# Performance work log

Measured on AMD Instinct MI355X. Metric: run time of the kernel, lower is better.

The kernel has to match this reference:

```python
import jax, jax.numpy as jnp
import numpy as np

N, B, E, H, G, L = 128, 2, 512, 1024, 50, 3
RBF_RADIUS = 12.0
AVG_LEN = 60.0


def _resmlp(h, Win, bin_, Wh, bh, Wout, bout):
    # input proj + activation, residual hidden blocks, linear head
    h = jax.nn.gelu(h @ Win + bin_, approximate=False)
    for i in range(Wh.shape[0]):  # fixed small number of layers
        h = h + jax.nn.gelu(h @ Wh[i] + bh[i], approximate=False)
    return h @ Wout + bout


def setup_inputs() -> dict:
    key = jax.random.key(0)
    ks = jax.random.split(key, 20)
    s_in = 1.0 / np.sqrt(3 * E)
    s_h = 1.0 / np.sqrt(H)
    s_g = 1.0 / np.sqrt(G)
    return {
        'x': jax.random.normal(ks[0], (N, B, E), jnp.float32),
        'dist': jax.random.uniform(ks[1], (N, N, B), jnp.float32),
        'vec_hat': jax.random.normal(ks[2], (N, N, B, 3), jnp.float32),
        'mask': jnp.ones((B, N), dtype=bool),
        'rbf_W': jax.random.normal(ks[3], (G, E), jnp.float32) * s_g,
        'rbf_b': jnp.zeros((E,), jnp.float32),
        'e_Win': jax.random.normal(ks[4], (3 * E, H), jnp.float32) * s_in,
        'e_bin': jnp.zeros((H,), jnp.float32),
        'e_Wh': jax.random.normal(ks[5], (L, H, H), jnp.float32) * s_h,
        'e_bh': jnp.zeros((L, H), jnp.float32),
        'e_Wout': jax.random.normal(ks[6], (H, 1), jnp.float32) * s_h,
        'e_bout': jnp.zeros((1,), jnp.float32),
        'f_Win': jax.random.normal(ks[7], (3 * E, H), jnp.float32) * s_in,
        'f_bin': jnp.zeros((H,), jnp.float32),
        'f_Wh': jax.random.normal(ks[8], (L, H, H), jnp.float32) * s_h,
        'f_bh': jnp.zeros((L, H), jnp.float32),
        'f_Wout': jax.random.normal(ks[9], (H, 1), jnp.float32) * s_h,
        'f_bout': jnp.zeros((1,), jnp.float32),
    }


def reference(x, dist, vec_hat, mask, rbf_W, rbf_b, e_Win, e_bin, e_Wh, e_bh,
              e_Wout, e_bout, f_Win, f_bin, f_Wh, f_bh, f_Wout, f_bout):
    # Gaussian RBF expansion + linear projection to embed_dim
    offset = jnp.linspace(0.0, RBF_RADIUS, G)
    coeff = -0.5 / (offset[1] - offset[0]) ** 2
    g = jnp.exp(coeff * (dist[..., None] - offset) ** 2)       # (N,N,B,G)
    rbf = g @ rbf_W + rbf_b                                    # (N,N,B,E)

    # all-pairs concat feature: [x_i, x_j, rbf_ij]  -> (N,N,B,3E)
    feat = jnp.concatenate([
        jnp.broadcast_to(x[:, None], rbf.shape),
        jnp.broadcast_to(x[None, :], rbf.shape),
        rbf,
    ], axis=-1)

    entries = (mask.T[:, None] & mask.T[None, :])[..., None].astype(feat.dtype)  # (N,N,B,1)

    energy_pairs = _resmlp(feat, e_Win, e_bin, e_Wh, e_bh, e_Wout, e_bout)       # (N,N,B,1)
    force_pairs = _resmlp(feat, f_Win, f_bin, f_Wh, f_bh, f_Wout, f_bout) * vec_hat  # (N,N,B,3)

    energy = (energy_pairs * entries).sum((0, 1)) / AVG_LEN ** 2  # (B,1)
    forces = (force_pairs * entries).sum(0) / AVG_LEN             # (N,B,3)
    # torch: forces.transpose(0,1)[mask]; mask is all-True here, so this is a reshape
    forces = jnp.swapaxes(forces, 0, 1).reshape(-1, 3)            # (B*N,3)
    return energy, forces
```

## Files before the change

### kernel.cpp

```cpp
#include <hip/hip_runtime.h>
#include <stdint.h>

typedef __bf16 bf16x8 __attribute__((ext_vector_type(8)));
typedef __bf16 bf16x4 __attribute__((ext_vector_type(4)));
typedef float  f32x4  __attribute__((ext_vector_type(4)));
typedef unsigned int u32;

__device__ __forceinline__ void gl_lds16(const void* gptr, void* lptr) {
    __builtin_amdgcn_global_load_lds(
        (const __attribute__((address_space(1))) u32*)gptr,
        (__attribute__((address_space(3))) u32*)lptr,
        16, 0, 0);
}

__device__ __forceinline__ float gelu_f(float x) {
    float u = 0.7978845608f * x * (1.0f + 0.044715f * x * x);
    float e = __expf(2.0f * u);
    float t = 1.0f - 2.0f / (e + 1.0f);
    return 0.5f * x * (1.0f + t);
}

#define MEMFENCE __asm__ __volatile__("" ::: "memory")

__global__ void zero_out(float* __restrict__ o, int n) {
    int i = blockIdx.x * 256 + threadIdx.x;
    if (i < n) o[i] = 0.0f;
}

__global__ __launch_bounds__(256)
void transpose_multi(const float* __restrict__ src0, const float* __restrict__ src1,
                     __bf16* __restrict__ dst0, __bf16* __restrict__ dst1,
                     int K, int Ncols, int perBranch) {
    const int z = blockIdx.z;
    const int branch = z / perBranch;
    const int l = z - branch * perBranch;
    const size_t elems = (size_t)K * Ncols;
    const float* src = (branch ? src1 : src0) + (size_t)l * elems;
    __bf16* dst = (branch ? dst1 : dst0) + (size_t)l * elems;

    __shared__ float tile[64][65];
    const int bk = blockIdx.x * 64;
    const int bn = blockIdx.y * 64;
    const int tid = threadIdx.x;
    const int tr = tid >> 4;
    const int tc = (tid & 15) * 4;
#pragma unroll
    for (int p = 0; p < 4; ++p) {
        const int r = tr + p * 16;
        float4 v = *(const float4*)&src[(size_t)(bk + r) * Ncols + bn + tc];
        tile[r][tc] = v.x; tile[r][tc + 1] = v.y;
        tile[r][tc + 2] = v.z; tile[r][tc + 3] = v.w;
    }
    __syncthreads();
#pragma unroll
    for (int p = 0; p < 4; ++p) {
        const int rn = tr + p * 16;
        bf16x4 o;
        o[0] = (__bf16)tile[tc + 0][rn];
        o[1] = (__bf16)tile[tc + 1][rn];
        o[2] = (__bf16)tile[tc + 2][rn];
        o[3] = (__bf16)tile[tc + 3][rn];
        *(bf16x4*)&dst[(size_t)(bn + rn) * K + bk + tc] = o;
    }
}

__global__ void f32_to_bf16(const float* __restrict__ s, __bf16* __restrict__ d, int n) {
    int idx = blockIdx.x * 256 + threadIdx.x;
    if (idx * 4 < n) {
        float4 v = *(const float4*)(s + idx * 4);
        bf16x4 o;
        o[0] = (__bf16)v.x; o[1] = (__bf16)v.y; o[2] = (__bf16)v.z; o[3] = (__bf16)v.w;
        *(bf16x4*)(d + idx * 4) = o;
    }
}

__global__ void build_M1(const float* __restrict__ rbfW, const float* __restrict__ rbf_b,
                         __bf16* __restrict__ M1) {
    int t = blockIdx.x * 256 + threadIdx.x;
    int r = t >> 8;
    int c = (t & 255) * 2;
    float v0 = 0.f, v1 = 0.f;
    if (r < 50)       { v0 = rbfW[r * 512 + c]; v1 = rbfW[r * 512 + c + 1]; }
    else if (r == 50) { v0 = rbf_b[c];          v1 = rbf_b[c + 1]; }
    M1[r * 512 + c] = (__bf16)v0;
    M1[r * 512 + c + 1] = (__bf16)v1;
}

__global__ __launch_bounds__(256)
void build_G(const float* __restrict__ dist, __bf16* __restrict__ G) {
    const int t = threadIdx.x;
    const int row = blockIdx.x * 32 + (t >> 3);
    const int c0 = (t & 7) * 8;
    const float sp = 12.0f / 49.0f;
    const float coeff = -0.5f / (sp * sp);
    const float d = dist[row];
    bf16x8 v;
#pragma unroll
    for (int q = 0; q < 8; ++q) {
        const int k = c0 + q;
        float val;
        if (k < 50)       { float tt = d - (float)k * sp; val = __expf(coeff * tt * tt); }
        else if (k == 50) val = 1.0f;
        else              val = 0.0f;
        v[q] = (__bf16)val;
    }
    *(bf16x8*)(G + (size_t)row * 64 + c0) = v;
}

template <int NK, int NBN, int MODE, bool DUAL, int MINW, bool SWZ>
__global__ __launch_bounds__(256, MINW)
void gemm_k(const __bf16* __restrict__ A0, const __bf16* __restrict__ A1,
            const __bf16* __restrict__ B0, const __bf16* __restrict__ B1,
            int lda, int ldb, int ldc,
            const float* __restrict__ bias0, const float* __restrict__ bias1,
            __bf16* __restrict__ C0, __bf16* __restrict__ C1,
            float* __restrict__ Cf0, float* __restrict__ Cf1,
            const float* __restrict__ P0, const float* __restrict__ P1,
            const float* __restrict__ wout0, const float* __restrict__ wout1,
            float* __restrict__ dot0, float* __restrict__ dot1) {
    constexpr int NBS = (NBN == 16) ? 4 : (NBN == 8) ? 3 : 0;
    __shared__ __align__(16) __bf16 As[3][128 * 32];
    __shared__ __align__(16) __bf16 Bs[3][128 * 32];

    const int tid = threadIdx.x;
    int bn, bm, branch = 0;
    if constexpr (SWZ) {
        const int x = blockIdx.x & 7;
        const int slot = blockIdx.x >> 3;
        bn = slot & (NBN - 1);
        int grp = x + ((slot >> NBS) << 3);
        if constexpr (DUAL) {
            const int half = (gridDim.x >> NBS) >> 1;
            branch = (grp >= half);
            if (branch) grp -= half;
        }
        bm = grp;
    } else {
        int f2 = blockIdx.x;
        if constexpr (DUAL) {
            const int half = gridDim.x >> 1;
            branch = (f2 >= half);
            if (branch) f2 -= half;
        }
        bn = f2 & (NBN - 1);
        bm = f2 >> NBS;
    }
    const int w = tid >> 6;
    const int lane = tid & 63;

    const __bf16* Ab = (DUAL && branch) ? A1 : A0;
    const __bf16* Bb = (DUAL && branch) ? B1 : B0;

    const int r0 = tid >> 2;
    const int s0 = tid & 3;
    const char* gA0 = (const char*)Ab + (size_t)(bm * 128 + r0) * lda + s0 * 16;
    const char* gA1 = gA0 + (size_t)64 * lda;
    const char* gB0 = (const char*)Bb + (size_t)(bn * 128 + r0) * ldb + s0 * 16;
    const char* gB1 = gB0 + (size_t)64 * ldb;

    char* lA0 = (char*)&As[0][0] + w * 1024;
    char* lA1 = (char*)&As[1][0] + w * 1024;
    char* lA2 = (char*)&As[2][0] + w * 1024;
    char* lB0 = (char*)&Bs[0][0] + w * 1024;
    char* lB1 = (char*)&Bs[1][0] + w * 1024;
    char* lB2 = (char*)&Bs[2][0] + w * 1024;

    const int wm = (w >> 1) & 1;
    const int wn = w & 1;
    const int lm = lane & 15;
    const int ko = (lane >> 4) << 3;
    const int fo = (wm * 64 + lm) * 32 + ko;
    const int go = (wn * 64 + lm) * 32 + ko;
    const __bf16* pA0 = &As[0][0] + fo;
    const __bf16* pA1 = &As[1][0] + fo;
    const __bf16* pA2 = &As[2][0] + fo;
    const __bf16* pB0 = &Bs[0][0] + go;
    const __bf16* pB1 = &Bs[1][0] + go;
    const __bf16* pB2 = &Bs[2][0] + go;

    f32x4 acc[4][4];
    const f32x4 zero = {0.0f, 0.0f, 0.0f, 0.0f};
#pragma unroll
    for (int i = 0; i < 4; ++i)
#pragma unroll
        for (int j = 0; j < 4; ++j) acc[i][j] = zero;

    auto stage = [&](int buf) {
        char* la = (buf == 0) ? lA0 : (buf == 1) ? lA1 : lA2;
        char* lb = (buf == 0) ? lB0 : (buf == 1) ? lB1 : lB2;
        gl_lds16(gA0, la); gl_lds16(gA1, la + 4096);
        gl_lds16(gB0, lb); gl_lds16(gB1, lb + 4096);
        gA0 += 64; gA1 += 64; gB0 += 64; gB1 += 64;
    };
    auto compute = [&](int buf) {
        const __bf16* pa = (buf == 0) ? pA0 : (buf == 1) ? pA1 : pA2;
        const __bf16* pb = (buf == 0) ? pB0 : (buf == 1) ? pB1 : pB2;
        bf16x8 af[4], bfg[4];
#pragma unroll
        for (int i = 0; i < 4; ++i) {
            af[i]  = *(const bf16x8*)(pa + i * 512);
            bfg[i] = *(const bf16x8*)(pb + i * 512);
        }
#pragma unroll
        for (int mi = 0; mi < 4; ++mi)
#pragma unroll
            for (int ni = 0; ni < 4; ++ni)
                acc[mi][ni] = __builtin_amdgcn_mfma_f32_16x16x32_bf16(
                    af[mi], bfg[ni], acc[mi][ni], 0, 0, 0);
    };
    auto iterstep = [&](int cbuf, int sbuf) {
        MEMFENCE;
        __builtin_amdgcn_s_waitcnt(0xF74);
        __builtin_amdgcn_s_barrier();
        MEMFENCE;
        compute(cbuf);
        MEMFENCE;
        stage(sbuf);
        MEMFENCE;
    };

    stage(0);
    stage(1);
    constexpr int NIT = NK - 2;
    constexpr int NG = NIT / 3;
    constexpr int NR = NIT % 3;
    for (int g = 0; g < NG; ++g) {
        iterstep(0, 2);
        iterstep(1, 0);
        iterstep(2, 1);
    }
    if constexpr (NR >= 1) iterstep(0, 2);
    if constexpr (NR >= 2) iterstep(1, 0);
    MEMFENCE;
    __builtin_amdgcn_s_waitcnt(0xF74);
    __builtin_amdgcn_s_barrier();
    MEMFENCE;
    compute((NK - 2) % 3);
    MEMFENCE;
    __builtin_amdgcn_s_waitcnt(0xF70);
    __builtin_amdgcn_s_barrier();
    MEMFENCE;
    compute((NK - 1) % 3);

    const int col0 = bn * 128 + wn * 64 + lm;
    const int row0 = bm * 128 + wm * 64 + ((lane >> 4) << 2);
    const int ldaE = lda >> 1;

    float rowdot[16];
    if constexpr (MODE == 1) {
#pragma unroll
        for (int q = 0; q < 16; ++q) rowdot[q] = 0.0f;
    }

    const bool side = (MODE == 2) && (bn >= 8);
    const float* bp = (MODE == 2) ? (side ? bias1 : bias0)
                                  : ((DUAL && branch) ? bias1 : bias0);
    __bf16* Cout = (MODE == 2) ? (side ? C1 : C0)
                               : ((DUAL && branch) ? C1 : C0);
    const float* woutb = (MODE == 1) ? ((DUAL && branch) ? wout1 : wout0) : nullptr;

#pragma unroll
    for (int ni = 0; ni < 4; ++ni) {
        const int gn = col0 + ni * 16;
        const int gnl = (MODE == 2) ? (gn & 1023) : gn;
        float bv = 0.0f;
        if constexpr (MODE <= 2) bv = bp[gnl];
        float wv = 0.0f;
        if constexpr (MODE == 1) wv = woutb[gn];

        float res[16];
        if constexpr (MODE == 0 || MODE == 1) {
#pragma unroll
            for (int mi = 0; mi < 4; ++mi)
#pragma unroll
                for (int rr = 0; rr < 4; ++rr)
                    res[mi * 4 + rr] =
                        (float)Ab[(size_t)(row0 + mi * 16 + rr) * ldaE + gn];
        } else if constexpr (MODE == 2) {
#pragma unroll
            for (int mi = 0; mi < 4; ++mi)
#pragma unroll
                for (int rr = 0; rr < 4; ++rr) {
                    const int gm = row0 + mi * 16 + rr;
                    const int p0row = ((gm >> 8) << 1) | (gm & 1);
                    const int p1row = gm & 255;
                    res[mi * 4 + rr] = P0[(size_t)p0row * 2048 + gn]
                                     + P1[(size_t)p1row * 2048 + gn];
                }
        }
        MEMFENCE;

#pragma unroll
        for (int mi = 0; mi < 4; ++mi) {
#pragma unroll
            for (int rr = 0; rr < 4; ++rr) {
                const int gm = row0 + mi * 16 + rr;
                const float a = acc[mi][ni][rr];
                if constexpr (MODE == 0) {
                    float v = gelu_f(a + bv) + res[mi * 4 + rr];
                    Cout[(size_t)gm * ldc + gn] = (__bf16)v;
                } else if constexpr (MODE == 1) {
                    float v = gelu_f(a + bv) + res[mi * 4 + rr];
                    rowdot[mi * 4 + rr] += v * wv;
                } else if constexpr (MODE == 2) {
                    float v = a + bv + res[mi * 4 + rr];
                    Cout[(size_t)gm * ldc + gnl] = (__bf16)gelu_f(v);
                } else if constexpr (MODE == 3) {
                    float* Cfw = (DUAL && branch) ? Cf1 : Cf0;
                    Cfw[(size_t)gm * ldc + gn] = a;
                } else {
                    C0[(size_t)gm * ldc + gn] = (__bf16)a;
                }
            }
        }
    }

    if constexpr (MODE == 1) {
#pragma unroll
        for (int s = 1; s < 16; s <<= 1)
#pragma unroll
            for (int q = 0; q < 16; ++q) rowdot[q] += __shfl_xor(rowdot[q], s);
        if (lm == 0) {
            float* dotb = (DUAL && branch) ? dot1 : dot0;
            float* dp = dotb + (size_t)(bn * 2 + wn) * 32768 + row0;
#pragma unroll
            for (int q = 0; q < 16; ++q)
                dp[(q >> 2) * 16 + (q & 3)] = rowdot[q];
        }
    }
}

#define WBAR(imm) do { MEMFENCE; __builtin_amdgcn_s_waitcnt(imm); \
                       __builtin_amdgcn_s_barrier(); MEMFENCE; } while (0)

template <int MODE, bool DUAL, int NBN, int NT, int LDA, int LDB>
__global__ __launch_bounds__(512, 2)
void gemm256(const __bf16* __restrict__ A0, const __bf16* __restrict__ A1,
             const __bf16* __restrict__ B0, const __bf16* __restrict__ B1,
             const float* __restrict__ bias0, const float* __restrict__ bias1,
             __bf16* __restrict__ C0, __bf16* __restrict__ C1,
             const float* __restrict__ wout0, const float* __restrict__ wout1,
             float* __restrict__ dot0, float* __restrict__ dot1,
             const float* __restrict__ P0, const float* __restrict__ P1) {
    constexpr int NBUF = (NT >= 3) ? 4 : 2;
    constexpr int NBS = (NBN == 8) ? 3 : 2;
    __shared__ __align__(16) char ldsbuf[NBUF * 32768];

    const int tid = threadIdx.x;
    const int nxg = gridDim.x >> 3;
    const int id = (blockIdx.x & 7) * nxg + (blockIdx.x >> 3);
    const int bn = id & (NBN - 1);
    int rest = id >> NBS;
    int branch = 0;
    if constexpr (DUAL) { branch = rest >> 7; rest &= 127; }
    const int bm = rest;

    const __bf16* __restrict__ Ab = (DUAL && branch) ? A1 : A0;
    const __bf16* __restrict__ Bb = (DUAL && branch) ? B1 : B0;

    const int w = tid >> 6;
    const int lane = tid & 63;

    const int srow = tid >> 2;
    const int scol = ((tid & 3) << 4) ^ (((tid >> 3) & 3) << 4);
    const char* gA = (const char*)Ab + (size_t)(bm * 256 + srow) * LDA + scol;
    const char* gB = (const char*)Bb + (size_t)(bn * 256 + srow) * LDB + scol;

    auto stageA = [&](int kt, int buf) {
        const size_t ko = (size_t)kt * 64;
        char* d = ldsbuf + buf * 32768 + w * 1024;
        gl_lds16(gA + ko,             d);
        gl_lds16(gA + ko + 128 * LDA, d + 8192);
    };
    auto stageB = [&](int kt, int buf) {
        const size_t ko = (size_t)kt * 64;
        char* d = ldsbuf + buf * 32768 + w * 1024;
        gl_lds16(gB + ko,             d + 16384);
        gl_lds16(gB + ko + 128 * LDB, d + 24576);
    };

    const int wm = w >> 2, wn = w & 3;
    const int lm = lane & 15, lq = lane >> 4;
    const int swz = ((lm >> 1) & 3) << 4;
    const int rA = (wm * 128 + lm) * 64 + ((lq * 16) ^ swz);
    const int rB = 16384 + (wn * 64 + lm) * 64 + ((lq * 16) ^ swz);

    f32x4 acc[4][8];
    const f32x4 zero = {0.0f, 0.0f, 0.0f, 0.0f};
#pragma unroll
    for (int i = 0; i < 4; ++i)
#pragma unroll
        for (int j = 0; j < 8; ++j) acc[i][j] = zero;

    auto body = [&](int kt, int cbuf, int sbuf, bool dostage) {
        const char* Lb = ldsbuf + cbuf * 32768;
        MEMFENCE;
        bf16x8 a[8], b[4];
#pragma unroll
        for (int ni = 0; ni < 4; ++ni)
            b[ni] = *(const bf16x8*)(Lb + rB + ni * 1024);
#pragma unroll
        for (int mi = 0; mi < 4; ++mi)
            a[mi] = *(const bf16x8*)(Lb + rA + mi * 1024);
        if (dostage) stageA(kt + 3, sbuf);
        MEMFENCE;
        __builtin_amdgcn_s_waitcnt(0xC07F);
        MEMFENCE;
        __builtin_amdgcn_s_setprio(1);
#pragma unroll
        for (int ni = 0; ni < 4; ++ni)
#pragma unroll
            for (int mi = 0; mi < 4; ++mi)
                acc[ni][mi] = __builtin_amdgcn_mfma_f32_16x16x32_bf16(
                    b[ni], a[mi], acc[ni][mi], 0, 0, 0);
        __builtin_amdgcn_s_setprio(0);
        __builtin_amdgcn_s_barrier();
        MEMFENCE;
#pragma unroll
        for (int mi = 4; mi < 8; ++mi)
            a[mi] = *(const bf16x8*)(Lb + rA + mi * 1024);
        if (dostage) stageB(kt + 3, sbuf);
        MEMFENCE;
        __builtin_amdgcn_s_waitcnt(0xC07F);
        MEMFENCE;
        __builtin_amdgcn_s_setprio(1);
#pragma unroll
        for (int ni = 0; ni < 4; ++ni)
#pragma unroll
            for (int mi = 4; mi < 8; ++mi)
                acc[ni][mi] = __builtin_amdgcn_mfma_f32_16x16x32_bf16(
                    b[ni], a[mi], acc[ni][mi], 0, 0, 0);
        __builtin_amdgcn_s_setprio(0);
    };

    if constexpr (NT == 32) {
        stageA(0, 0); stageB(0, 0);
        stageA(1, 1); stageB(1, 1);
        stageA(2, 2); stageB(2, 2);
        for (int g = 0; g < 7; ++g) {
            const int k0 = g * 4;
            WBAR(0xF78); body(k0 + 0, 0, 3, true);
            WBAR(0xF78); body(k0 + 1, 1, 0, true);
            WBAR(0xF78); body(k0 + 2, 2, 1, true);
            WBAR(0xF78); body(k0 + 3, 3, 2, true);
        }
        WBAR(0xF78); body(28, 0, 3, true);
        WBAR(0xF78); body(29, 1, 0, false);
        WBAR(0xF74); body(30, 2, 1, false);
        WBAR(0xF70); body(31, 3, 2, false);
    } else {
        stageA(0, 0); stageB(0, 0);
        stageA(1, 1); stageB(1, 1);
        WBAR(0xF74); body(0, 0, 0, false);
        WBAR(0xF70); body(1, 1, 0, false);
    }

    const int rowb = bm * 256 + wm * 128 + lm;
    const int nbase = bn * 256 + wn * 64 + lq * 4;

    if constexpr (MODE == 2) {
        const bool side = (bn >= (NBN >> 1));
        const float* __restrict__ bp = side ? bias1 : bias0;
        __bf16* __restrict__ Cw = side ? C1 : C0;
        const int nloc = nbase & 1023;
        f32x4 bv[4], p0v[4];
        const size_t p0base = (size_t)((bm << 1) | (lm & 1)) * 2048;
#pragma unroll
        for (int ni = 0; ni < 4; ++ni) {
            bv[ni]  = *(const f32x4*)&bp[nloc + ni * 16];
            p0v[ni] = *(const f32x4*)&P0[p0base + nbase + ni * 16];
        }
#pragma unroll
        for (int mi = 0; mi < 8; ++mi) {
            const int p1row = wm * 128 + mi * 16 + lm;
            f32x4 p1v[4];
#pragma unroll
            for (int ni = 0; ni < 4; ++ni)
                p1v[ni] = *(const f32x4*)&P1[(size_t)p1row * 2048 + nbase + ni * 16];
            MEMFENCE;
            const size_t rb = (size_t)(rowb + mi * 16) * 1024;
#pragma unroll
            for (int ni = 0; ni < 4; ++ni) {
                bf16x4 o;
#pragma unroll
                for (int r = 0; r < 4; ++r)
                    o[r] = (__bf16)gelu_f(acc[ni][mi][r] + bv[ni][r] +
                                          p0v[ni][r] + p1v[ni][r]);
                *(bf16x4*)&Cw[rb + nloc + ni * 16] = o;
            }
        }
        return;
    }

    const float* __restrict__ bp = (DUAL && branch) ? bias1 : bias0;
    f32x4 bv[4];
#pragma unroll
    for (int ni = 0; ni < 4; ++ni)
        bv[ni] = *(const f32x4*)&bp[nbase + ni * 16];

    if constexpr (MODE == 0) {
        __bf16* __restrict__ Cw = (DUAL && branch) ? C1 : C0;
#pragma unroll
        for (int mi = 0; mi < 8; ++mi) {
            const size_t rb = (size_t)(rowb + mi * 16) * 1024;
            bf16x4 res[4];
#pragma unroll
            for (int ni = 0; ni < 4; ++ni)
                res[ni] = *(const bf16x4*)&Ab[rb + nbase + ni * 16];
            MEMFENCE;
#pragma unroll
            for (int ni = 0; ni < 4; ++ni) {
                bf16x4 o;
#pragma unroll
                for (int r = 0; r < 4; ++r)
                    o[r] = (__bf16)(gelu_f(acc[ni][mi][r] + bv[ni][r]) +
                                    (float)res[ni][r]);
                *(bf16x4*)&Cw[rb + nbase + ni * 16] = o;
            }
        }
    } else if constexpr (MODE == 1) {
        const float* __restrict__ wb = (DUAL && branch) ? wout1 : wout0;
        f32x4 wv[4];
#pragma unroll
        for (int ni = 0; ni < 4; ++ni)
            wv[ni] = *(const f32x4*)&wb[nbase + ni * 16];
        float rd[8];
#pragma unroll
        for (int q = 0; q < 8; ++q) rd[q] = 0.0f;
#pragma unroll
        for (int mi = 0; mi < 8; ++mi) {
            const size_t rb = (size_t)(rowb + mi * 16) * 1024;
            bf16x4 res[4];
#pragma unroll
            for (int ni = 0; ni < 4; ++ni)
                res[ni] = *(const bf16x4*)&Ab[rb + nbase + ni * 16];
            MEMFENCE;
#pragma unroll
            for (int ni = 0; ni < 4; ++ni)
#pragma unroll
                for (int r = 0; r < 4; ++r) {
                    float v = gelu_f(acc[ni][mi][r] + bv[ni][r]) +
                              (float)res[ni][r];
                    rd[mi] += v * wv[ni][r];
                }
        }
#pragma unroll
        for (int mi = 0; mi < 8; ++mi) {
            rd[mi] += __shfl_xor(rd[mi], 16);
            rd[mi] += __shfl_xor(rd[mi], 32);
        }
        if (lq == 0) {
            float* __restrict__ db = (DUAL && branch) ? dot1 : dot0;
            float* dp = db + (size_t)(bn * 4 + wn) * 32768 + bm * 256 + wm * 128;
#pragma unroll
            for (int mi = 0; mi < 8; ++mi)
                dp[mi * 16 + lm] = rd[mi];
        }
    }
}

__global__ __launch_bounds__(128)
void finalize(const float* __restrict__ dot_e, const float* __restrict__ dot_f,
              const float* __restrict__ eb, const float* __restrict__ fb,
              const float* __restrict__ vec, float* __restrict__ out) {
    const int bj = blockIdx.x;
    const int bb = bj >> 7, jj = bj & 127;
    const int i = threadIdx.x;
    const int m = (i * 128 + jj) * 2 + bb;
    float e = eb[0], f = fb[0];
#pragma unroll
    for (int s = 0; s < 16; ++s) {
        e += dot_e[(size_t)s * 32768 + m];
        f += dot_f[(size_t)s * 32768 + m];
    }
    f *= (1.0f / 60.0f);
    float fx = f * vec[(size_t)m * 3 + 0];
    float fy = f * vec[(size_t)m * 3 + 1];
    float fz = f * vec[(size_t)m * 3 + 2];
#pragma unroll
    for (int off = 32; off > 0; off >>= 1) {
        e  += __shfl_down(e, off);
        fx += __shfl_down(fx, off);
        fy += __shfl_down(fy, off);
        fz += __shfl_down(fz, off);
    }
    __shared__ float red[2][4];
    const int wv = i >> 6, lane = i & 63;
    if (lane == 0) { red[wv][0] = e; red[wv][1] = fx; red[wv][2] = fy; red[wv][3] = fz; }
    __syncthreads();
    if (i == 0) {
        atomicAdd(&out[bb], (red[0][0] + red[1][0]) * (1.0f / 3600.0f));
        float* fo = out + 2 + bj * 3;
        fo[0] = red[0][1] + red[1][1];
        fo[1] = red[0][2] + red[1][2];
        fo[2] = red[0][3] + red[1][3];
    }
}

extern "C" void kernel_launch(void* const* d_in, const int* in_sizes, int n_in,
                              void* d_out, int out_size, void* d_ws, size_t ws_size,
                              hipStream_t stream) {
    const float* x     = (const float*)d_in[0];
    const float* dist  = (const float*)d_in[1];
    const float* vec   = (const float*)d_in[2];
    const float* rbfW  = (const float*)d_in[4];
    const float* rbf_b = (const float*)d_in[5];
    const float* eWin  = (const float*)d_in[6];
    const float* ebin  = (const float*)d_in[7];
    const float* eWh   = (const float*)d_in[8];
    const float* ebh   = (const float*)d_in[9];
    const float* eWout = (const float*)d_in[10];
    const float* ebout = (const float*)d_in[11];
    const float* fWin  = (const float*)d_in[12];
    const float* fbin  = (const float*)d_in[13];
    const float* fWh   = (const float*)d_in[14];
    const float* fbh   = (const float*)d_in[15];
    const float* fWout = (const float*)d_in[16];
    const float* fbout = (const float*)d_in[17];
    float* out = (float*)d_out;

    char* p = (char*)d_ws;
    __bf16* WinTcat = (__bf16*)p;
    __bf16* eWinT = WinTcat;          p += (size_t)1024 * 1536 * 2;
    __bf16* fWinT = (__bf16*)p;       p += (size_t)1024 * 1536 * 2;
    __bf16* eWhT0 = (__bf16*)p;       p += (size_t)3 * 1024 * 1024 * 2;
    __bf16* fWhT0 = (__bf16*)p;       p += (size_t)3 * 1024 * 1024 * 2;
    __bf16* xb  = (__bf16*)p;         p += (size_t)256 * 512 * 2;
    __bf16* M1  = (__bf16*)p;         p += (size_t)128 * 512 * 2;
    __bf16* WgT = (__bf16*)p;         p += (size_t)2048 * 128 * 2;
    __bf16* G   = (__bf16*)p;         p += (size_t)32768 * 64 * 2;
    float* P0   = (float*)p;          p += (size_t)256 * 2048 * 4;
    float* P1   = (float*)p;          p += (size_t)256 * 2048 * 4;
    float* dot_e = (float*)p;         p += (size_t)16 * 32768 * 4;
    float* dot_f = (float*)p;         p += (size_t)16 * 32768 * 4;
    const size_t SLAB = (size_t)32768 * 1024 * 2;
    __bf16* he0 = (__bf16*)p;         p += SLAB;
    __bf16* hf0 = (__bf16*)p;         p += SLAB;
    __bf16* hAe = (__bf16*)p;         p += SLAB;
    __bf16* hAf = hAe;
    const bool dualHidden = ((size_t)(p - (char*)d_ws) + SLAB) <= ws_size;
    if (dualHidden) hAf = (__bf16*)p;

    zero_out<<<dim3(4), dim3(256), 0, stream>>>(out, 770);

    transpose_multi<<<dim3(24, 16, 2), dim3(256), 0, stream>>>(
        eWin, fWin, eWinT, fWinT, 1536, 1024, 1);
    transpose_multi<<<dim3(16, 16, 6), dim3(256), 0, stream>>>(
        eWh, fWh, eWhT0, fWhT0, 1024, 1024, 3);
    f32_to_bf16<<<dim3(128), dim3(256), 0, stream>>>(x, xb, 131072);
    build_M1<<<dim3(128), dim3(256), 0, stream>>>(rbfW, rbf_b, M1);
    build_G<<<dim3(1024), dim3(256), 0, stream>>>(dist, G);

    const dim3 blk(256);
    gemm_k<16, 16, 3, true, 3, false><<<dim3(64), blk, 0, stream>>>(
        xb, xb, WinTcat, WinTcat + 512, 1024, 3072, 2048,
        nullptr, nullptr, nullptr, nullptr, P0, P1,
        nullptr, nullptr, nullptr, nullptr, nullptr, nullptr);
    gemm_k<16, 1, 4, false, 3, false><<<dim3(16), blk, 0, stream>>>(
        WinTcat + 1024, nullptr, M1, nullptr, 3072, 1024, 128,
        nullptr, nullptr, WgT, nullptr, nullptr, nullptr,
        nullptr, nullptr, nullptr, nullptr, nullptr, nullptr);

    const dim3 blk512(512);
    gemm256<2, false, 8, 2, 128, 256><<<dim3(1024), blk512, 0, stream>>>(
        G, nullptr, WgT, nullptr, ebin, fbin, he0, hf0,
        nullptr, nullptr, nullptr, nullptr, P0, P1);

    if (dualHidden) {
        gemm256<0, true, 4, 32, 2048, 2048><<<dim3(1024), blk512, 0, stream>>>(
            he0, hf0, eWhT0, fWhT0, ebh + 0, fbh + 0,
            hAe, hAf, nullptr, nullptr, nullptr, nullptr, nullptr, nullptr);
        gemm256<0, true, 4, 32, 2048, 2048><<<dim3(1024), blk512, 0, stream>>>(
            hAe, hAf, eWhT0 + (size_t)1048576, fWhT0 + (size_t)1048576,
            ebh + 1024, fbh + 1024, he0, hf0,
            nullptr, nullptr, nullptr, nullptr, nullptr, nullptr);
        gemm256<1, true, 4, 32, 2048, 2048><<<dim3(1024), blk512, 0, stream>>>(
            he0, hf0, eWhT0 + (size_t)2 * 1048576, fWhT0 + (size_t)2 * 1048576,
            ebh + 2048, fbh + 2048, nullptr, nullptr,
            eWout, fWout, dot_e, dot_f, nullptr, nullptr);
    } else {
        gemm256<0, false, 4, 32, 2048, 2048><<<dim3(512), blk512, 0, stream>>>(
            he0, nullptr, eWhT0, nullptr, ebh + 0, nullptr,
            hAe, nullptr, nullptr, nullptr, nullptr, nullptr, nullptr, nullptr);
        gemm256<0, false, 4, 32, 2048, 2048><<<dim3(512), blk512, 0, stream>>>(
            hAe, nullptr, eWhT0 + (size_t)1048576, nullptr, ebh + 1024, nullptr,
            he0, nullptr, nullptr, nullptr, nullptr, nullptr, nullptr, nullptr);
        gemm256<1, false, 4, 32, 2048, 2048><<<dim3(512), blk512, 0, stream>>>(
            he0, nullptr, eWhT0 + (size_t)2 * 1048576, nullptr, ebh + 2048, nullptr,
            nullptr, nullptr, eWout, nullptr, dot_e, nullptr, nullptr, nullptr);
        gemm256<0, false, 4, 32, 2048, 2048><<<dim3(512), blk512, 0, stream>>>(
            hf0, nullptr, fWhT0, nullptr, fbh + 0, nullptr,
            hAf, nullptr, nullptr, nullptr, nullptr, nullptr, nullptr, nullptr);
        gemm256<0, false, 4, 32, 2048, 2048><<<dim3(512), blk512, 0, stream>>>(
            hAf, nullptr, fWhT0 + (size_t)1048576, nullptr, fbh + 1024, nullptr,
            hf0, nullptr, nullptr, nullptr, nullptr, nullptr, nullptr, nullptr);
        gemm256<1, false, 4, 32, 2048, 2048><<<dim3(512), blk512, 0, stream>>>(
            hf0, nullptr, fWhT0 + (size_t)2 * 1048576, nullptr, fbh + 2048, nullptr,
            nullptr, nullptr, fWout, nullptr, dot_f, nullptr, nullptr, nullptr);
    }

    finalize<<<dim3(256), dim3(128), 0, stream>>>(dot_e, dot_f, ebout, fbout, vec, out);
}
```

Baseline: 706.4 us.

## Merge prep kernels and add two-buffer pipeline variant for first hidden GEMM

Folds the zero-fill, bf16 casts, M1 build and RBF basis construction into one prep kernel, and both weight transposes into a single launch, to cut launch overhead. Adds a PIPE2 variant of the 256-tile GEMM that double-buffers LDS with a barrier after the fragment reads, so more workgroups can be resident (launch bounds raised to 4). Only the first dual hidden-layer GEMM uses it, which reads like an A/B test. The small-K path also switches to the new body. Fewer in-flight stages may expose memory latency, and a minimum of 4 workgroups of 512 threads caps registers per thread, which could cause spills.

```diff
diff --git a/kernel.cpp b/kernel.cpp
--- a/kernel.cpp
+++ b/kernel.cpp
@@ -22,25 +22,75 @@
 
 #define MEMFENCE __asm__ __volatile__("" ::: "memory")
 
-__global__ void zero_out(float* __restrict__ o, int n) {
-    int i = blockIdx.x * 256 + threadIdx.x;
-    if (i < n) o[i] = 0.0f;
+__global__ __launch_bounds__(256)
+void prep_all(const float* __restrict__ dist, __bf16* __restrict__ G,
+              const float* __restrict__ x, __bf16* __restrict__ xb,
+              const float* __restrict__ rbfW, const float* __restrict__ rbf_b,
+              __bf16* __restrict__ M1, float* __restrict__ out) {
+    const int b = blockIdx.x;
+    const int t = threadIdx.x;
+    if (b < 1024) {
+        const int row = b * 32 + (t >> 3);
+        const int c0 = (t & 7) * 8;
+        const float sp = 12.0f / 49.0f;
+        const float coeff = -0.5f / (sp * sp);
+        const float d = dist[row];
+        bf16x8 v;
+#pragma unroll
+        for (int q = 0; q < 8; ++q) {
+            const int k = c0 + q;
+            float val;
+            if (k < 50)       { float tt = d - (float)k * sp; val = __expf(coeff * tt * tt); }
+            else if (k == 50) val = 1.0f;
+            else              val = 0.0f;
+            v[q] = (__bf16)val;
+        }
+        *(bf16x8*)(G + (size_t)row * 64 + c0) = v;
+    } else if (b < 1152) {
+        const int idx = (b - 1024) * 256 + t;
+        float4 v = *(const float4*)(x + idx * 4);
+        bf16x4 o;
+        o[0] = (__bf16)v.x; o[1] = (__bf16)v.y; o[2] = (__bf16)v.z; o[3] = (__bf16)v.w;
+        *(bf16x4*)(xb + idx * 4) = o;
+    } else if (b < 1280) {
+        const int tt = (b - 1152) * 256 + t;
+        const int r = tt >> 8;
+        const int c = (tt & 255) * 2;
+        float v0 = 0.f, v1 = 0.f;
+        if (r < 50)       { v0 = rbfW[r * 512 + c]; v1 = rbfW[r * 512 + c + 1]; }
+        else if (r == 50) { v0 = rbf_b[c];          v1 = rbf_b[c + 1]; }
+        M1[r * 512 + c] = (__bf16)v0;
+        M1[r * 512 + c + 1] = (__bf16)v1;
+    } else {
+        const int i = (b - 1280) * 256 + t;
+        if (i < 770) out[i] = 0.0f;
+    }
 }
 
 __global__ __launch_bounds__(256)
-void transpose_multi(const float* __restrict__ src0, const float* __restrict__ src1,
-                     __bf16* __restrict__ dst0, __bf16* __restrict__ dst1,
-                     int K, int Ncols, int perBranch) {
+void transpose_all(const float* __restrict__ eWin, const float* __restrict__ fWin,
+                   __bf16* __restrict__ eWinT, __bf16* __restrict__ fWinT,
+                   const float* __restrict__ eWh, const float* __restrict__ fWh,
+                   __bf16* __restrict__ eWhT, __bf16* __restrict__ fWhT) {
     const int z = blockIdx.z;
-    const int branch = z / perBranch;
-    const int l = z - branch * perBranch;
-    const size_t elems = (size_t)K * Ncols;
-    const float* src = (branch ? src1 : src0) + (size_t)l * elems;
-    __bf16* dst = (branch ? dst1 : dst0) + (size_t)l * elems;
+    int K, branch, l;
+    const float* src;
+    __bf16* dst;
+    if (z < 2) {
+        K = 1536; branch = z; l = 0;
+        src = branch ? fWin : eWin;
+        dst = branch ? fWinT : eWinT;
+    } else {
+        K = 1024; const int zz = z - 2; branch = zz / 3; l = zz - branch * 3;
+        src = (branch ? fWh : eWh) + (size_t)l * 1024 * 1024;
+        dst = (branch ? fWhT : eWhT) + (size_t)l * 1024 * 1024;
+    }
+    const int Ncols = 1024;
+    const int bk = blockIdx.x * 64;
+    if (bk >= K) return;
+    const int bn = blockIdx.y * 64;
 
     __shared__ float tile[64][65];
-    const int bk = blockIdx.x * 64;
-    const int bn = blockIdx.y * 64;
     const int tid = threadIdx.x;
     const int tr = tid >> 4;
     const int tc = (tid & 15) * 4;
@@ -62,49 +112,6 @@
         o[3] = (__bf16)tile[tc + 3][rn];
         *(bf16x4*)&dst[(size_t)(bn + rn) * K + bk + tc] = o;
     }
-}
-
-__global__ void f32_to_bf16(const float* __restrict__ s, __bf16* __restrict__ d, int n) {
-    int idx = blockIdx.x * 256 + threadIdx.x;
-    if (idx * 4 < n) {
-        float4 v = *(const float4*)(s + idx * 4);
-        bf16x4 o;
-        o[0] = (__bf16)v.x; o[1] = (__bf16)v.y; o[2] = (__bf16)v.z; o[3] = (__bf16)v.w;
-        *(bf16x4*)(d + idx * 4) = o;
-    }
-}
-
-__global__ void build_M1(const float* __restrict__ rbfW, const float* __restrict__ rbf_b,
-                         __bf16* __restrict__ M1) {
-    int t = blockIdx.x * 256 + threadIdx.x;
-    int r = t >> 8;
-    int c = (t & 255) * 2;
-    float v0 = 0.f, v1 = 0.f;
-    if (r < 50)       { v0 = rbfW[r * 512 + c]; v1 = rbfW[r * 512 + c + 1]; }
-    else if (r == 50) { v0 = rbf_b[c];          v1 = rbf_b[c + 1]; }
-    M1[r * 512 + c] = (__bf16)v0;
-    M1[r * 512 + c + 1] = (__bf16)v1;
-}
-
-__global__ __launch_bounds__(256)
-void build_G(const float* __restrict__ dist, __bf16* __restrict__ G) {
-    const int t = threadIdx.x;
-    const int row = blockIdx.x * 32 + (t >> 3);
-    const int c0 = (t & 7) * 8;
-    const float sp = 12.0f / 49.0f;
-    const float coeff = -0.5f / (sp * sp);
-    const float d = dist[row];
-    bf16x8 v;
-#pragma unroll
-    for (int q = 0; q < 8; ++q) {
-        const int k = c0 + q;
-        float val;
-        if (k < 50)       { float tt = d - (float)k * sp; val = __expf(coeff * tt * tt); }
-        else if (k == 50) val = 1.0f;
-        else              val = 0.0f;
-        v[q] = (__bf16)val;
-    }
-    *(bf16x8*)(G + (size_t)row * 64 + c0) = v;
 }
 
 template <int NK, int NBN, int MODE, bool DUAL, int MINW, bool SWZ>
@@ -333,8 +340,8 @@
 #define WBAR(imm) do { MEMFENCE; __builtin_amdgcn_s_waitcnt(imm); \
                        __builtin_amdgcn_s_barrier(); MEMFENCE; } while (0)
 
-template <int MODE, bool DUAL, int NBN, int NT, int LDA, int LDB>
-__global__ __launch_bounds__(512, 2)
+template <int MODE, bool DUAL, int NBN, int NT, int LDA, int LDB, bool PIPE2>
+__global__ __launch_bounds__(512, PIPE2 ? 4 : 2)
 void gemm256(const __bf16* __restrict__ A0, const __bf16* __restrict__ A1,
              const __bf16* __restrict__ B0, const __bf16* __restrict__ B1,
              const float* __restrict__ bias0, const float* __restrict__ bias1,
@@ -342,7 +349,7 @@
              const float* __restrict__ wout0, const float* __restrict__ wout1,
              float* __restrict__ dot0, float* __restrict__ dot1,
              const float* __restrict__ P0, const float* __restrict__ P1) {
-    constexpr int NBUF = (NT >= 3) ? 4 : 2;
+    constexpr int NBUF = PIPE2 ? 2 : ((NT >= 3) ? 4 : 2);
     constexpr int NBS = (NBN == 8) ? 3 : 2;
     __shared__ __align__(16) char ldsbuf[NBUF * 32768];
 
@@ -433,7 +440,34 @@
         __builtin_amdgcn_s_setprio(0);
     };
 
-    if constexpr (NT == 32) {
+    auto body2 = [&](int kt, int buf, bool dostage) {
+        const char* Lb = ldsbuf + buf * 32768;
+        MEMFENCE;
+        bf16x8 a[8], b[4];
+#pragma unroll
+        for (int ni = 0; ni < 4; ++ni)
+            b[ni] = *(const bf16x8*)(Lb + rB + ni * 1024);
+#pragma unroll
+        for (int mi = 0; mi < 8; ++mi)
+            a[mi] = *(const bf16x8*)(Lb + rA + mi * 1024);
+        MEMFENCE;
+        __builtin_amdgcn_s_waitcnt(0xC07F);
+        MEMFENCE;
+        __builtin_amdgcn_s_barrier();
+        MEMFENCE;
+        if (dostage) { stageA(kt + 2, buf); stageB(kt + 2, buf); }
+        MEMFENCE;
+        __builtin_amdgcn_s_setprio(1);
+#pragma unroll
+        for (int ni = 0; ni < 4; ++ni)
+#pragma unroll
+            for (int mi = 0; mi < 8; ++mi)
+                acc[ni][mi] = __builtin_amdgcn_mfma_f32_16x16x32_bf16(
+                    b[ni], a[mi], acc[ni][mi], 0, 0, 0);
+        __builtin_amdgcn_s_setprio(0);
+    };
+
+    if constexpr (NT == 32 && !PIPE2) {
         stageA(0, 0); stageB(0, 0);
         stageA(1, 1); stageB(1, 1);
         stageA(2, 2); stageB(2, 2);
@@ -448,11 +482,20 @@
         WBAR(0xF78); body(29, 1, 0, false);
         WBAR(0xF74); body(30, 2, 1, false);
         WBAR(0xF70); body(31, 3, 2, false);
+    } else if constexpr (NT == 32 && PIPE2) {
+        stageA(0, 0); stageB(0, 0);
+        stageA(1, 1); stageB(1, 1);
+        for (int g = 0; g < 15; ++g) {
+            WBAR(0xF74); body2(2 * g + 0, 0, true);
+            WBAR(0xF74); body2(2 * g + 1, 1, true);
+        }
+        WBAR(0xF74); body2(30, 0, false);
+        WBAR(0xF70); body2(31, 1, false);
     } else {
         stageA(0, 0); stageB(0, 0);
         stageA(1, 1); stageB(1, 1);
-        WBAR(0xF74); body(0, 0, 0, false);
-        WBAR(0xF70); body(1, 1, 0, false);
+        WBAR(0xF74); body2(0, 0, false);
+        WBAR(0xF70); body2(1, 1, false);
     }
 
     const int rowb = bm * 256 + wm * 128 + lm;
@@ -641,15 +684,10 @@
     const bool dualHidden = ((size_t)(p - (char*)d_ws) + SLAB) <= ws_size;
     if (dualHidden) hAf = (__bf16*)p;
 
-    zero_out<<<dim3(4), dim3(256), 0, stream>>>(out, 770);
-
-    transpose_multi<<<dim3(24, 16, 2), dim3(256), 0, stream>>>(
-        eWin, fWin, eWinT, fWinT, 1536, 1024, 1);
-    transpose_multi<<<dim3(16, 16, 6), dim3(256), 0, stream>>>(
-        eWh, fWh, eWhT0, fWhT0, 1024, 1024, 3);
-    f32_to_bf16<<<dim3(128), dim3(256), 0, stream>>>(x, xb, 131072);
-    build_M1<<<dim3(128), dim3(256), 0, stream>>>(rbfW, rbf_b, M1);
-    build_G<<<dim3(1024), dim3(256), 0, stream>>>(dist, G);
+    prep_all<<<dim3(1284), dim3(256), 0, stream>>>(
+        dist, G, x, xb, rbfW, rbf_b, M1, out);
+    transpose_all<<<dim3(24, 16, 8), dim3(256), 0, stream>>>(
+        eWin, fWin, eWinT, fWinT, eWh, fWh, eWhT0, fWhT0);
 
     const dim3 blk(256);
     gemm_k<16, 16, 3, true, 3, false><<<dim3(64), blk, 0, stream>>>(
@@ -662,39 +700,39 @@
         nullptr, nullptr, nullptr, nullptr, nullptr, nullptr);
 
     const dim3 blk512(512);
-    gemm256<2, false, 8, 2, 128, 256><<<dim3(1024), blk512, 0, stream>>>(
+    gemm256<2, false, 8, 2, 128, 256, false><<<dim3(1024), blk512, 0, stream>>>(
         G, nullptr, WgT, nullptr, ebin, fbin, he0, hf0,
         nullptr, nullptr, nullptr, nullptr, P0, P1);
 
     if (dualHidden) {
-        gemm256<0, true, 4, 32, 2048, 2048><<<dim3(1024), blk512, 0, stream>>>(
+        gemm256<0, true, 4, 32, 2048, 2048, true><<<dim3(1024), blk512, 0, stream>>>(
             he0, hf0, eWhT0, fWhT0, ebh + 0, fbh + 0,
             hAe, hAf, nullptr, nullptr, nullptr, nullptr, nullptr, nullptr);
-        gemm256<0, true, 4, 32, 2048, 2048><<<dim3(1024), blk512, 0, stream>>>(
+        gemm256<0, true, 4, 32, 2048, 2048, false><<<dim3(1024), blk512, 0, stream>>>(
             hAe, hAf, eWhT0 + (size_t)1048576, fWhT0 + (size_t)1048576,
             ebh + 1024, fbh + 1024, he0, hf0,
             nullptr, nullptr, nullptr, nullptr, nullptr, nullptr);
-        gemm256<1, true, 4, 32, 2048, 2048><<<dim3(1024), blk512, 0, stream>>>(
+        gemm256<1, true, 4, 32, 2048, 2048, false><<<dim3(1024), blk512, 0, stream>>>(
             he0, hf0, eWhT0 + (size_t)2 * 1048576, fWhT0 + (size_t)2 * 1048576,
             ebh + 2048, fbh + 2048, nullptr, nullptr,
             eWout, fWout, dot_e, dot_f, nullptr, nullptr);
     } else {
-        gemm256<0, false, 4, 32, 2048, 2048><<<dim3(512), blk512, 0, stream>>>(
+        gemm256<0, false, 4, 32, 2048, 2048, false><<<dim3(512), blk512, 0, stream>>>(
             he0, nullptr, eWhT0, nullptr, ebh + 0, nullptr,
             hAe, nullptr, nullptr, nullptr, nullptr, nullptr, nullptr, nullptr);
-        gemm256<0, false, 4, 32, 2048, 2048><<<dim3(512), blk512, 0, stream>>>(
+        gemm256<0, false, 4, 32, 2048, 2048, false><<<dim3(512), blk512, 0, stream>>>(
             hAe, nullptr, eWhT0 + (size_t)1048576, nullptr, ebh + 1024, nullptr,
             he0, nullptr, nullptr, nullptr, nullptr, nullptr, nullptr, nullptr);
-        gemm256<1, false, 4, 32, 2048, 2048><<<dim3(512), blk512, 0, stream>>>(
+        gemm256<1, false, 4, 32, 2048, 2048, false><<<dim3(512), blk512, 0, stream>>>(
             he0, nullptr, eWhT0 + (size_t)2 * 1048576, nullptr, ebh + 2048, nullptr,
             nullptr, nullptr, eWout, nullptr, dot_e, nullptr, nullptr, nullptr);
-        gemm256<0, false, 4, 32, 2048, 2048><<<dim3(512), blk512, 0, stream>>>(
+        gemm256<0, false, 4, 32, 2048, 2048, false><<<dim3(512), blk512, 0, stream>>>(
             hf0, nullptr, fWhT0, nullptr, fbh + 0, nullptr,
             hAf, nullptr, nullptr, nullptr, nullptr, nullptr, nullptr, nullptr);
-        gemm256<0, false, 4, 32, 2048, 2048><<<dim3(512), blk512, 0, stream>>>(
+        gemm256<0, false, 4, 32, 2048, 2048, false><<<dim3(512), blk512, 0, stream>>>(
             hAf, nullptr, fWhT0 + (size_t)1048576, nullptr, fbh + 1024, nullptr,
             hf0, nullptr, nullptr, nullptr, nullptr, nullptr, nullptr, nullptr);
-        gemm256<1, false, 4, 32, 2048, 2048><<<dim3(512), blk512, 0, stream>>>(
+        gemm256<1, false, 4, 32, 2048, 2048, false><<<dim3(512), blk512, 0, stream>>>(
             hf0, nullptr, fWhT0 + (size_t)2 * 1048576, nullptr, fbh + 2048, nullptr,
             nullptr, nullptr, fWout, nullptr, dot_f, nullptr, nullptr, nullptr);
     }
```

Result: slower. 729.8 us (+3.3%).
